# Performance work log

Measured on AMD Instinct MI355X. Metric: run time of the kernel, lower is better.

Reference implementation:

```python
import jax, jax.numpy as jnp
import numpy as np

N = 512      # nodes
F_IN = 16    # raw node features; adjacency channels = 2*F_IN = 32
H = 64       # hidden
HF = 64      # hidden_final
C = 10       # num_classes
L = 3        # num_layers
E = 16384    # edges (avg degree 32)
EPS = 1e-5


def setup_inputs() -> dict:
    key = jax.random.key(0)
    ks = iter(jax.random.split(key, 40))
    rn = lambda shape, s=0.05: jax.random.normal(next(ks), shape, jnp.float32) * s
    inp = {
        'x': jax.random.normal(next(ks), (N, F_IN), jnp.float32),
        'edge_index': jax.random.randint(next(ks), (2, E), 0, N),
        # no_prop FeatureExtractor
        'np1_w': rn((HF, 2 * F_IN)), 'np1_b': rn((HF,)),
        'np2_w': rn((HF, 2 * F_IN)), 'np3_w': rn((HF, HF)),
        # first PowerfulLayer (in = 2*F_IN)
        'c0_m1_w': rn((H, 2 * F_IN)), 'c0_m1_b': rn((H,)),
        'c0_m2_w': rn((H, 2 * F_IN)), 'c0_m2_b': rn((H,)),
        'c0_m4_w': rn((H, 2 * F_IN + H)), 'c0_m4_b': rn((H,)),
        # remaining L-1 PowerfulLayers (stacked)
        'cm1_w': rn((L - 1, H, H)), 'cm1_b': rn((L - 1, H)),
        'cm2_w': rn((L - 1, H, H)), 'cm2_b': rn((L - 1, H)),
        'cm4_w': rn((L - 1, H, 2 * H)), 'cm4_b': rn((L - 1, H)),
        # batchnorms (training-mode stats; affine params)
        'bn_g': jnp.ones((L, H), jnp.float32), 'bn_b': jnp.zeros((L, H), jnp.float32),
        # per-layer FeatureExtractors (stacked)
        'fe1_w': rn((L, HF, H)), 'fe1_b': rn((L, HF)),
        'fe2_w': rn((L, HF, H)), 'fe3_w': rn((L, HF, HF)),
        # after_conv and final linear
        'ac_w': rn((HF, HF)), 'ac_b': rn((HF,)),
        'fl_w': rn((C, HF)), 'fl_b': rn((C,)),
    }
    return inp


def _lin(x, w, b=None):
    y = x @ w.T
    return y if b is None else y + b


def _extractor(u, w1, b1, w2, w3):
    # u: [B, N, N, F]; graph_class=True, aggr='add'
    n = u.shape[1]
    trace = jnp.einsum('biif->bf', u)                     # sum of diagonal entries
    out1 = _lin(trace / n, w1, b1)
    s = (u.sum(axis=(1, 2)) - trace) / (n * (n - 1))      # off-diagonal mean-ish
    out = out1 + _lin(s, w2)
    return out + _lin(jax.nn.relu(out), w3)


def _powerful(u, m1w, m1b, m2w, m2b, m4w, m4b):
    # UnitMLP with 1 layer == 1x1 conv == per-position linear (no ReLU)
    o1 = jnp.einsum('bijc,oc->bijo', u, m1w) + m1b        # [B,N,N,H]
    o2 = jnp.einsum('bijc,oc->bijo', u, m2w) + m2b
    mult = jnp.einsum('bikh,bkjh->bijh', o1, o2)          # per-channel NxN matmul
    return _lin(jnp.concatenate([mult, u], axis=-1), m4w, m4b)


def _batchnorm(u, g, b):
    # BatchNorm2d in training mode: stats over (batch, N, N) per channel, biased var
    mean = u.mean(axis=(0, 1, 2))
    var = u.var(axis=(0, 1, 2))
    return (u - mean) * jax.lax.rsqrt(var + EPS) * g + b


def reference(x, edge_index, np1_w, np1_b, np2_w, np3_w,
              c0_m1_w, c0_m1_b, c0_m2_w, c0_m2_b, c0_m4_w, c0_m4_b,
              cm1_w, cm1_b, cm2_w, cm2_b, cm4_w, cm4_b,
              bn_g, bn_b, fe1_w, fe1_b, fe2_w, fe3_w,
              ac_w, ac_b, fl_w, fl_b):
    n = x.shape[0]
    src, dst = edge_index[0], edge_index[1]
    edge_attr = jnp.concatenate([x[src], x[dst]], axis=-1)          # [E, 2F]
    A = jnp.zeros((n, n, edge_attr.shape[-1]), x.dtype).at[src, dst].add(edge_attr)
    u = A[None]                                                      # [1,N,N,2F]

    out = _extractor(u, np1_w, np1_b, np2_w, np3_w)
    nlayers = bn_g.shape[0]
    for l in range(nlayers):
        if l == 0:
            u = _powerful(u, c0_m1_w, c0_m1_b, c0_m2_w, c0_m2_b, c0_m4_w, c0_m4_b)
        else:
            u = _powerful(u, cm1_w[l - 1], cm1_b[l - 1], cm2_w[l - 1], cm2_b[l - 1],
                          cm4_w[l - 1], cm4_b[l - 1])
        u = _batchnorm(u, bn_g[l], bn_b[l])
        out = out + _extractor(u, fe1_w[l], fe1_b[l], fe2_w[l], fe3_w[l])

    out = jax.nn.relu(out) / nlayers
    out = out + jax.nn.relu(_lin(out, ac_w, ac_b))   # layer_after_conv
    # dropout with p=0.0 / eval mode is identity
    out = _lin(out, fl_w, fl_b)
    return jax.nn.log_softmax(out, axis=-1)          # [1, num_classes]
```

## Files before the change

### kernel.cpp

```cpp
#include <hip/hip_runtime.h>
#include <hip/hip_bf16.h>

#define Nn   512
#define NN   262144
#define EDG  16384

typedef unsigned short u16;
typedef short v8s __attribute__((ext_vector_type(8)));
typedef float v4f __attribute__((ext_vector_type(4)));
typedef u16 u16x8 __attribute__((ext_vector_type(8)));

__device__ __forceinline__ float b2f(u16 u) {
    union { unsigned int i; float f; } v; v.i = ((unsigned int)u) << 16; return v.f;
}
__device__ __forceinline__ u16 f2b(float f) {
    union { float f; unsigned int i; } v; v.f = f;
    unsigned int r = (v.i + 0x7FFFu + ((v.i >> 16) & 1u)) >> 16;
    return (u16)r;
}

__global__ void sentinel_kernel(float* __restrict__ out, float val) {
    if (threadIdx.x < 10) out[threadIdx.x] = val;
}

__global__ void cvt_weights(const float* __restrict__ s0, const float* __restrict__ s1,
                            const float* __restrict__ s2, const float* __restrict__ s3,
                            const float* __restrict__ s4, const float* __restrict__ s5,
                            u16* __restrict__ dst) {
    int t = blockIdx.x * 256 + threadIdx.x;
    if (t >= 43008) return;
    float v;
    if      (t < 2048)  v = s0[t];
    else if (t < 4096)  v = s1[t - 2048];
    else if (t < 10240) v = s2[t - 4096];
    else if (t < 18432) v = s3[t - 10240];
    else if (t < 26624) v = s4[t - 18432];
    else                v = s5[t - 26624];
    dst[t] = f2b(v);
}

__global__ void scatter_edges(const float* __restrict__ x, const int* __restrict__ ei,
                              float* __restrict__ A) {
    int t = blockIdx.x * 256 + threadIdx.x;
    if (t >= EDG * 32) return;
    int e = t >> 5, c = t & 31;
    int s = ei[e], d = ei[EDG + e];
    float v = (c < 16) ? x[s * 16 + c] : x[d * 16 + (c - 16)];
    atomicAdd(A + ((size_t)s * Nn + d) * 32 + c, v);
}

__global__ __launch_bounds__(256) void finalize_u0(const float* __restrict__ A,
                                                   u16* __restrict__ u0,
                                                   float* __restrict__ total) {
    __shared__ u16 L[32 * 258];
    __shared__ float red[4][32];
    int t = threadIdx.x;
    int p0 = blockIdx.x * 256;
    const float* Ar = A + (size_t)(p0 + t) * 32;
    float v[32];
#pragma unroll
    for (int c = 0; c < 32; ++c) v[c] = Ar[c];
#pragma unroll
    for (int c = 0; c < 32; ++c) L[c * 258 + t] = f2b(v[c]);
    int wv = t >> 6;
#pragma unroll
    for (int c = 0; c < 32; ++c) {
        float r = v[c];
        for (int off = 32; off > 0; off >>= 1) r += __shfl_down(r, off);
        if ((t & 63) == 0) red[wv][c] = r;
    }
    __syncthreads();
    if (t < 32) atomicAdd(total + t, red[0][t] + red[1][t] + red[2][t] + red[3][t]);
    int off = (t & 31) * 8, rb = t >> 5;
#pragma unroll
    for (int pass = 0; pass < 4; ++pass) {
        int c = pass * 8 + rb;
        u16x8 w = *(const u16x8*)(L + c * 258 + off);
        *(u16x8*)(u0 + (size_t)c * NN + p0 + off) = w;
    }
}

__global__ void trace_raw_cm(const u16* __restrict__ ucm, float* __restrict__ trraw) {
    int c = blockIdx.x, t = threadIdx.x;
    const u16* base = ucm + (size_t)c * NN;
    float s = b2f(base[(size_t)(2 * t) * 513]) + b2f(base[(size_t)(2 * t + 1) * 513]);
    for (int off = 32; off > 0; off >>= 1) s += __shfl_down(s, off);
    __shared__ float r[4];
    if ((t & 63) == 0) r[t >> 6] = s;
    __syncthreads();
    if (t == 0) trraw[c] = r[0] + r[1] + r[2] + r[3];
}

template<int NCH>
__global__ __launch_bounds__(256) void conv12_t(
    const u16* __restrict__ src,
    const float* __restrict__ sc, const float* __restrict__ sh,
    const u16* __restrict__ w1, const float* __restrict__ b1,
    const u16* __restrict__ w2, const float* __restrict__ b2,
    u16* __restrict__ dst1, u16* __restrict__ dst2)
{
    __shared__ u16 LS[8320];
    const int C = NCH * 32;
    const int t = threadIdx.x;
    const int P0 = blockIdx.x * 128;
    const int lane = t & 63, wave = t >> 6;
    const int l15 = lane & 15, quad = lane >> 4;
    const int pw = wave * 32;
    const int sr = t >> 4;
    const int so = (t & 15) * 8;

    u16x8 pf[NCH][2];
#pragma unroll
    for (int kc = 0; kc < NCH; ++kc)
#pragma unroll
        for (int ps = 0; ps < 2; ++ps)
            pf[kc][ps] = *(const u16x8*)(src + (size_t)(kc * 32 + ps * 16 + sr) * NN + P0 + so);

    v4f acc[2][4][2];
#pragma unroll
    for (int s = 0; s < 2; ++s)
#pragma unroll
        for (int mt = 0; mt < 4; ++mt)
#pragma unroll
            for (int nt = 0; nt < 2; ++nt) acc[s][mt][nt] = (v4f){0.f, 0.f, 0.f, 0.f};

    {
        u16* Ln = LS;
#pragma unroll
        for (int ps = 0; ps < 2; ++ps) {
            int c = ps * 16 + sr;
            u16x8 v = pf[0][ps];
            if (sc) {
                float s = sc[c], f = sh[c];
#pragma unroll
                for (int j = 0; j < 8; ++j) v[j] = f2b(b2f(v[j]) * s + f);
            }
            *(u16x8*)(Ln + c * 130 + so) = v;
        }
    }
    __syncthreads();
#pragma unroll
    for (int kc = 0; kc < NCH; ++kc) {
        if (kc + 1 < NCH) {
            u16* Ln = LS + ((kc + 1) & 1) * 4160;
#pragma unroll
            for (int ps = 0; ps < 2; ++ps) {
                int c = ps * 16 + sr;
                int cg = (kc + 1) * 32 + c;
                u16x8 v = pf[kc + 1][ps];
                if (sc) {
                    float s = sc[cg], f = sh[cg];
#pragma unroll
                    for (int j = 0; j < 8; ++j) v[j] = f2b(b2f(v[j]) * s + f);
                }
                *(u16x8*)(Ln + c * 130 + so) = v;
            }
        }
        v8s af1[4], af2[4];
#pragma unroll
        for (int mt = 0; mt < 4; ++mt) {
            af1[mt] = *(const v8s*)(w1 + (mt * 16 + l15) * C + kc * 32 + quad * 8);
            af2[mt] = *(const v8s*)(w2 + (mt * 16 + l15) * C + kc * 32 + quad * 8);
        }
        const u16* Lb = LS + (kc & 1) * 4160;
#pragma unroll
        for (int nt = 0; nt < 2; ++nt) {
            const int p = pw + nt * 16 + l15;
            v8s b;
#pragma unroll
            for (int j = 0; j < 8; ++j) b[j] = (short)Lb[(quad * 8 + j) * 130 + p];
#pragma unroll
            for (int mt = 0; mt < 4; ++mt) {
                acc[0][mt][nt] = __builtin_amdgcn_mfma_f32_16x16x32_bf16(af1[mt], b, acc[0][mt][nt], 0, 0, 0);
                acc[1][mt][nt] = __builtin_amdgcn_mfma_f32_16x16x32_bf16(af2[mt], b, acc[1][mt][nt], 0, 0, 0);
            }
        }
        if (kc + 1 < NCH) __syncthreads();
    }
#pragma unroll
    for (int s = 0; s < 2; ++s) {
        __syncthreads();
        const float* bb = s ? b2 : b1;
#pragma unroll
        for (int mt = 0; mt < 4; ++mt)
#pragma unroll
            for (int r = 0; r < 4; ++r) {
                const int h = mt * 16 + quad * 4 + r;
                const float bv = bb[h];
#pragma unroll
                for (int nt = 0; nt < 2; ++nt)
                    LS[h * 130 + pw + nt * 16 + l15] = f2b(acc[s][mt][nt][r] + bv);
            }
        __syncthreads();
        u16* dd = s ? dst2 : dst1;
#pragma unroll
        for (int ps = 0; ps < 4; ++ps) {
            int h = ps * 16 + sr;
            u16x8 v = *(const u16x8*)(LS + h * 130 + so);
            __builtin_nontemporal_store(v, (u16x8*)(dd + (size_t)h * NN + P0 + so));
        }
    }
}

template<int NCH>
__global__ __launch_bounds__(256) void conv4_t(
    const u16* __restrict__ mult, const u16* __restrict__ u,
    const float* __restrict__ sc, const float* __restrict__ sh,
    const u16* __restrict__ w, const float* __restrict__ bias,
    u16* __restrict__ dst,
    float* __restrict__ psum, float* __restrict__ psq, float* __restrict__ ptr)
{
    __shared__ u16 LS[8320];
    __shared__ float R1[64][4], R2[64][4];
    const int K = NCH * 32;
    const int t = threadIdx.x;
    const int P0 = blockIdx.x * 128;
    const int lane = t & 63, wave = t >> 6;
    const int l15 = lane & 15, quad = lane >> 4;
    const int pw = wave * 32;
    const int sr = t >> 4;
    const int so = (t & 15) * 8;

    u16x8 pf[NCH][2];
#pragma unroll
    for (int kc = 0; kc < NCH; ++kc)
#pragma unroll
        for (int ps = 0; ps < 2; ++ps) {
            int cg = kc * 32 + ps * 16 + sr;
            const u16* gp = (cg < 64) ? (mult + (size_t)cg * NN + P0 + so)
                                      : (u + (size_t)(cg - 64) * NN + P0 + so);
            pf[kc][ps] = *(const u16x8*)gp;
        }

    v4f acc[4][2];
#pragma unroll
    for (int mt = 0; mt < 4; ++mt)
#pragma unroll
        for (int nt = 0; nt < 2; ++nt) acc[mt][nt] = (v4f){0.f, 0.f, 0.f, 0.f};

#pragma unroll
    for (int ps = 0; ps < 2; ++ps)
        *(u16x8*)(LS + (ps * 16 + sr) * 130 + so) = pf[0][ps];
    __syncthreads();
#pragma unroll
    for (int kc = 0; kc < NCH; ++kc) {
        if (kc + 1 < NCH) {
            u16* Ln = LS + ((kc + 1) & 1) * 4160;
#pragma unroll
            for (int ps = 0; ps < 2; ++ps) {
                int c = ps * 16 + sr;
                int cg = (kc + 1) * 32 + c;
                u16x8 v = pf[kc + 1][ps];
                if (cg >= 64 && sc) {
                    float s = sc[cg - 64], f = sh[cg - 64];
#pragma unroll
                    for (int j = 0; j < 8; ++j) v[j] = f2b(b2f(v[j]) * s + f);
                }
                *(u16x8*)(Ln + c * 130 + so) = v;
            }
        }
        v8s af[4];
#pragma unroll
        for (int mt = 0; mt < 4; ++mt)
            af[mt] = *(const v8s*)(w + (mt * 16 + l15) * K + kc * 32 + quad * 8);
        const u16* Lb = LS + (kc & 1) * 4160;
#pragma unroll
        for (int nt = 0; nt < 2; ++nt) {
            const int p = pw + nt * 16 + l15;
            v8s b;
#pragma unroll
            for (int j = 0; j < 8; ++j) b[j] = (short)Lb[(quad * 8 + j) * 130 + p];
#pragma unroll
            for (int mt = 0; mt < 4; ++mt)
                acc[mt][nt] = __builtin_amdgcn_mfma_f32_16x16x32_bf16(af[mt], b, acc[mt][nt], 0, 0, 0);
        }
        if (kc + 1 < NCH) __syncthreads();
    }
    __syncthreads();
#pragma unroll
    for (int mt = 0; mt < 4; ++mt)
#pragma unroll
        for (int r = 0; r < 4; ++r) {
            const int h = mt * 16 + quad * 4 + r;
            const float bv = bias[h];
#pragma unroll
            for (int nt = 0; nt < 2; ++nt)
                LS[h * 130 + pw + nt * 16 + l15] = f2b(acc[mt][nt][r] + bv);
        }
    __syncthreads();
    {
        int c = t >> 2, q = t & 3;
        const u16* row = LS + c * 130 + q * 32;
        float s = 0.f, s2 = 0.f;
#pragma unroll
        for (int i = 0; i < 32; ++i) { float v = b2f(row[i]); s += v; s2 += v * v; }
        R1[c][q] = s; R2[c][q] = s2;
    }
    __syncthreads();
    {
        int i = P0 >> 9, j0 = P0 & 511;
        int blk = blockIdx.x;
        if (t < 64) {
            psum[t * 2048 + blk] = R1[t][0] + R1[t][1] + R1[t][2] + R1[t][3];
            psq[t * 2048 + blk]  = R2[t][0] + R2[t][1] + R2[t][2] + R2[t][3];
            if (j0 <= i && i < j0 + 128) ptr[t * 512 + i] = b2f(LS[t * 130 + (i - j0)]);
        }
    }
#pragma unroll
    for (int ps = 0; ps < 4; ++ps) {
        int h = ps * 16 + sr;
        u16x8 v = *(const u16x8*)(LS + h * 130 + so);
        __builtin_nontemporal_store(v, (u16x8*)(dst + (size_t)h * NN + P0 + so));
    }
}

__global__ __launch_bounds__(256) void bmm_mfma(const u16* __restrict__ Aall,
                                                const u16* __restrict__ Ball,
                                                u16* __restrict__ Call) {
    __shared__ u16 LA[128 * 72];
    __shared__ u16 LB[64 * 130];
    const int h = blockIdx.y;
    const int tx = blockIdx.x & 3, ty = blockIdx.x >> 2;
    const int t = threadIdx.x;
    const int lane = t & 63, wave = t >> 6;
    const int l15 = lane & 15, quad = lane >> 4;
    const int jb = wave * 32;
    const u16* Ap = Aall + (size_t)h * NN + (size_t)ty * 128 * 512;
    const u16* Bp = Ball + (size_t)h * NN + tx * 128;

    const int srow = t >> 3;
    const int scol = (t & 7) * 8;
    const int bkr = t >> 4;
    const int bjg = (t & 15) * 8;

    v4f acc[8][2];
#pragma unroll
    for (int mt = 0; mt < 8; ++mt)
#pragma unroll
        for (int nt = 0; nt < 2; ++nt) acc[mt][nt] = (v4f){0.f, 0.f, 0.f, 0.f};

    v8s ra[4], rb[4];
#pragma unroll
    for (int i = 0; i < 4; ++i) {
        ra[i] = *(const v8s*)(Ap + (size_t)(i * 32 + srow) * 512 + scol);
        rb[i] = *(const v8s*)(Bp + (size_t)(i * 16 + bkr) * 512 + bjg);
    }

    for (int ck = 0; ck < 8; ++ck) {
#pragma unroll
        for (int i = 0; i < 4; ++i) {
            *(v8s*)(LA + (i * 32 + srow) * 72 + scol) = ra[i];
            *(v8s*)(LB + (i * 16 + bkr) * 130 + bjg) = rb[i];
        }
        __syncthreads();
        if (ck < 7) {
            const int k0 = (ck + 1) * 64;
#pragma unroll
            for (int i = 0; i < 4; ++i) {
                ra[i] = *(const v8s*)(Ap + (size_t)(i * 32 + srow) * 512 + k0 + scol);
                rb[i] = *(const v8s*)(Bp + (size_t)(k0 + i * 16 + bkr) * 512 + bjg);
            }
        }
#pragma unroll
        for (int kk = 0; kk < 2; ++kk) {
            v8s b[2];
#pragma unroll
            for (int nt = 0; nt < 2; ++nt) {
                const int j = jb + nt * 16 + l15;
#pragma unroll
                for (int jj = 0; jj < 8; ++jj)
                    b[nt][jj] = (short)LB[(kk * 32 + quad * 8 + jj) * 130 + j];
            }
#pragma unroll
            for (int mh = 0; mh < 2; ++mh) {
                v8s a[4];
#pragma unroll
                for (int m = 0; m < 4; ++m)
                    a[m] = *(const v8s*)(LA + ((mh * 4 + m) * 16 + l15) * 72 + kk * 32 + quad * 8);
#pragma unroll
                for (int m = 0; m < 4; ++m)
#pragma unroll
                    for (int nt = 0; nt < 2; ++nt)
                        acc[mh * 4 + m][nt] = __builtin_amdgcn_mfma_f32_16x16x32_bf16(a[m], b[nt], acc[mh * 4 + m][nt], 0, 0, 0);
            }
        }
        __syncthreads();
    }

    u16* Cp = Call + (size_t)h * NN;
#pragma unroll
    for (int mt = 0; mt < 8; ++mt)
#pragma unroll
        for (int r = 0; r < 4; ++r) {
            const int i = ty * 128 + mt * 16 + quad * 4 + r;
#pragma unroll
            for (int nt = 0; nt < 2; ++nt) {
                const int j = tx * 128 + jb + nt * 16 + l15;
                Cp[i * 512 + j] = f2b(acc[mt][nt][r]);
            }
        }
}

__global__ __launch_bounds__(256) void bn_finalize(
    const float* __restrict__ psum, const float* __restrict__ psq,
    const float* __restrict__ ptr,
    const float* __restrict__ g, const float* __restrict__ b,
    float* __restrict__ scale, float* __restrict__ shift,
    float* __restrict__ ttl) {
    int c = blockIdx.x, t = threadIdx.x;
    float s = 0.f, q = 0.f, tr = 0.f;
    for (int k = t; k < 2048; k += 256) { s += psum[c * 2048 + k]; q += psq[c * 2048 + k]; }
    for (int k = t; k < 512; k += 256) tr += ptr[c * 512 + k];
    for (int off = 32; off > 0; off >>= 1) {
        s += __shfl_down(s, off); q += __shfl_down(q, off); tr += __shfl_down(tr, off);
    }
    __shared__ float r1[4], r2[4], r3[4];
    if ((t & 63) == 0) { r1[t >> 6] = s; r2[t >> 6] = q; r3[t >> 6] = tr; }
    __syncthreads();
    if (t == 0) {
        s = r1[0] + r1[1] + r1[2] + r1[3];
        q = r2[0] + r2[1] + r2[2] + r2[3];
        tr = r3[0] + r3[1] + r3[2] + r3[3];
        float mean = s * (1.f / 262144.f);
        float var = q * (1.f / 262144.f) - mean * mean;
        float sc = g[c] * rsqrtf(fmaxf(var, 0.f) + 1e-5f);
        float sh = b[c] - mean * sc;
        scale[c] = sc;
        shift[c] = sh;
        ttl[64 + c] = sc * s + 262144.f * sh;
        ttl[c]      = sc * tr + 512.f * sh;
    }
}

__global__ __launch_bounds__(256) void extractor_par(
    const float* __restrict__ tt,
    const float* __restrict__ np1w, const float* __restrict__ np1b,
    const float* __restrict__ np2w, const float* __restrict__ np3w,
    const float* __restrict__ fe1w, const float* __restrict__ fe1b,
    const float* __restrict__ fe2w, const float* __restrict__ fe3w,
    float* __restrict__ oacc_part) {
    __shared__ float red[64][4];
    __shared__ float xo[64];
    const int li = blockIdx.x;
    const int t = threadIdx.x;
    const int h = t >> 2, q = t & 3;
    const int C = (li == 0) ? 32 : 64;
    const float* w1 = (li == 0) ? np1w : fe1w + (li - 1) * 4096;
    const float* b1 = (li == 0) ? np1b : fe1b + (li - 1) * 64;
    const float* w2 = (li == 0) ? np2w : fe2w + (li - 1) * 4096;
    const float* w3 = (li == 0) ? np3w : fe3w + (li - 1) * 4096;
    const float* tr = tt + li * 128;
    const float* to = tr + 64;
    const int cpq = C >> 2;
    float p = 0.f;
    for (int i = 0; i < cpq; ++i) {
        int c = q * cpq + i;
        p += (tr[c] * (1.f / 512.f)) * w1[h * C + c]
           + ((to[c] - tr[c]) * (1.f / (512.f * 511.f))) * w2[h * C + c];
    }
    red[h][q] = p;
    __syncthreads();
    if (q == 0) xo[h] = b1[h] + red[h][0] + red[h][1] + red[h][2] + red[h][3];
    __syncthreads();
    float o = xo[h];
    float p3 = 0.f;
    for (int i = 0; i < 16; ++i) {
        int f = q * 16 + i;
        p3 += fmaxf(xo[f], 0.f) * w3[h * 64 + f];
    }
    __syncthreads();
    red[h][q] = p3;
    __syncthreads();
    if (q == 0) oacc_part[li * 64 + h] = o + red[h][0] + red[h][1] + red[h][2] + red[h][3];
}

__global__ __launch_bounds__(256) void head_par(
    const float* __restrict__ oacc_part,
    const float* __restrict__ acw, const float* __restrict__ acb,
    const float* __restrict__ flw, const float* __restrict__ flb,
    float* __restrict__ out) {
    __shared__ float x[64], x2[64], red[64][4], l[10];
    const int t = threadIdx.x;
    const int h = t >> 2, q = t & 3;
    if (q == 0) {
        float oa = oacc_part[h] + oacc_part[64 + h] + oacc_part[128 + h] + oacc_part[192 + h];
        x[h] = fmaxf(oa, 0.f) * (1.f / 3.f);
    }
    __syncthreads();
    float p = 0.f;
    for (int i = 0; i < 16; ++i) { int f = q * 16 + i; p += x[f] * acw[h * 64 + f]; }
    red[h][q] = p;
    __syncthreads();
    if (q == 0) {
        float y = acb[h] + red[h][0] + red[h][1] + red[h][2] + red[h][3];
        x2[h] = x[h] + fmaxf(y, 0.f);
    }
    __syncthreads();
    if (t < 40) {
        int hh = t >> 2, qq = t & 3;
        float p2 = 0.f;
        for (int i = 0; i < 16; ++i) { int f = qq * 16 + i; p2 += x2[f] * flw[hh * 64 + f]; }
        red[hh][qq] = p2;
    }
    __syncthreads();
    if (t < 10) l[t] = flb[t] + red[t][0] + red[t][1] + red[t][2] + red[t][3];
    __syncthreads();
    if (t == 0) {
        float m = l[0];
        for (int i = 1; i < 10; ++i) m = fmaxf(m, l[i]);
        float se = 0.f;
        for (int i = 0; i < 10; ++i) se += expf(l[i] - m);
        float ls = m + logf(se);
        for (int i = 0; i < 10; ++i) out[i] = l[i] - ls;
    }
}

extern "C" void kernel_launch(void* const* d_in, const int* in_sizes, int n_in,
                              void* d_out, int out_size, void* d_ws, size_t ws_size,
                              hipStream_t stream) {
    float* out = (float*)d_out;

    static const int exp_sizes[28] = {
        8192, 32768,
        2048, 64, 2048, 4096,
        2048, 64, 2048, 64, 6144, 64,
        8192, 128, 8192, 128, 16384, 128,
        192, 192,
        12288, 192, 12288, 12288,
        4096, 64, 640, 10
    };
    bool ok = (n_in == 28);
    if (ok) for (int i = 0; i < 28; ++i) if (in_sizes[i] != exp_sizes[i]) ok = false;
    if (!ok) { sentinel_kernel<<<1, 64, 0, stream>>>(out, -5.0f); return; }

    const size_t RSZ = (size_t)NN * 64 * 2;
    const size_t BIG_OFF = 8192 + 90112;
    if (ws_size < BIG_OFF + 4 * RSZ) {
        sentinel_kernel<<<1, 64, 0, stream>>>(out, -7.0f);
        return;
    }

    const float* x     = (const float*)d_in[0];
    const int*   ei    = (const int*)d_in[1];
    const float* np1w  = (const float*)d_in[2];
    const float* np1b  = (const float*)d_in[3];
    const float* np2w  = (const float*)d_in[4];
    const float* np3w  = (const float*)d_in[5];
    const float* c0m1b = (const float*)d_in[7];
    const float* c0m2b = (const float*)d_in[9];
    const float* c0m4b = (const float*)d_in[11];
    const float* cm1b  = (const float*)d_in[13];
    const float* cm2b  = (const float*)d_in[15];
    const float* cm4b  = (const float*)d_in[17];
    const float* bng   = (const float*)d_in[18];
    const float* bnb   = (const float*)d_in[19];
    const float* fe1w  = (const float*)d_in[20];
    const float* fe1b  = (const float*)d_in[21];
    const float* fe2w  = (const float*)d_in[22];
    const float* fe3w  = (const float*)d_in[23];
    const float* acw   = (const float*)d_in[24];
    const float* acb   = (const float*)d_in[25];
    const float* flw   = (const float*)d_in[26];
    const float* flb   = (const float*)d_in[27];

    char* ws = (char*)d_ws;
    float* small = (float*)ws;
    float* tt    = small;
    float* scl   = small + 512;
    float* shf   = small + 576;
    float* oaccp = small + 640;

    u16* arena = (u16*)(ws + 8192);

    char* big = ws + BIG_OFF;
    u16* S0 = (u16*)(big + 0 * RSZ);
    u16* S1 = (u16*)(big + 1 * RSZ);
    u16* S2 = (u16*)(big + 2 * RSZ);
    u16* S3 = (u16*)(big + 3 * RSZ);
    float* Abuf = (float*)S2;

    float* psum = (float*)S2;
    float* psq  = psum + 64 * 2048;
    float* ptr  = psq + 64 * 2048;

    hipMemsetAsync(small, 0, 4096, stream);
    hipMemsetAsync(Abuf, 0, (size_t)NN * 32 * 4, stream);

    cvt_weights<<<168, 256, 0, stream>>>((const float*)d_in[6], (const float*)d_in[8],
                                         (const float*)d_in[10], (const float*)d_in[12],
                                         (const float*)d_in[14], (const float*)d_in[16], arena);
    scatter_edges<<<2048, 256, 0, stream>>>(x, ei, Abuf);
    finalize_u0<<<1024, 256, 0, stream>>>(Abuf, S0, tt + 64);
    trace_raw_cm<<<32, 256, 0, stream>>>(S0, tt);

    u16* U[3]  = { S0, S1, S0 };
    u16* O1[3] = { S1, S0, S1 };
    u16* R[3]  = { S1, S0, S1 };

    const float *aff_s = nullptr, *aff_h = nullptr;

    for (int l = 0; l < 3; ++l) {
        int Cin = (l == 0) ? 32 : 64;
        const u16 *w1b, *w2b, *w4b;
        const float *b1, *b2, *b4;
        if (l == 0) {
            w1b = arena;            b1 = c0m1b;
            w2b = arena + 2048;     b2 = c0m2b;
            w4b = arena + 4096;     b4 = c0m4b;
        } else {
            int m = l - 1;
            w1b = arena + 10240 + m * 4096;  b1 = cm1b + m * 64;
            w2b = arena + 18432 + m * 4096;  b2 = cm2b + m * 64;
            w4b = arena + 26624 + m * 8192;  b4 = cm4b + m * 64;
        }
        if (Cin == 32)
            conv12_t<1><<<2048, 256, 0, stream>>>(U[l], aff_s, aff_h, w1b, b1, w2b, b2, O1[l], S2);
        else
            conv12_t<2><<<2048, 256, 0, stream>>>(U[l], aff_s, aff_h, w1b, b1, w2b, b2, O1[l], S2);
        bmm_mfma<<<dim3(16, 64), 256, 0, stream>>>(O1[l], S2, S3);
        if (Cin == 32)
            conv4_t<3><<<2048, 256, 0, stream>>>(S3, U[l], aff_s, aff_h, w4b, b4, R[l], psum, psq, ptr);
        else
            conv4_t<4><<<2048, 256, 0, stream>>>(S3, U[l], aff_s, aff_h, w4b, b4, R[l], psum, psq, ptr);
        bn_finalize<<<64, 256, 0, stream>>>(psum, psq, ptr, bng + l * 64, bnb + l * 64,
                                            scl, shf, tt + (l + 1) * 128);
        aff_s = scl; aff_h = shf;
    }
    extractor_par<<<4, 256, 0, stream>>>(tt, np1w, np1b, np2w, np3w,
                                         fe1w, fe1b, fe2w, fe3w, oaccp);
    head_par<<<1, 256, 0, stream>>>(oaccp, acw, acb, flw, flb, out);
}
```

Baseline: 471.1 us.

## Double-buffer B tile in LDS, read A directly from global, swap block order

The bmm kernel no longer stages the A tile in shared memory. Each wave loads its A fragments straight from global memory (L1/L2), and the B tile is double-buffered in LDS so each k-step needs one barrier instead of two. The block index mapping is also swapped so that neighbouring blocks share the same B column tile. This lowers LDS traffic and barrier count, at the cost of redundant global loads of A across waves and more exposed global memory latency inside the MFMA loop.

Result: slower. 630.0 us (+33.7%).

```diff
diff --git a/kernel.cpp b/kernel.cpp
--- a/kernel.cpp
+++ b/kernel.cpp
@@ -317,19 +317,15 @@
 __global__ __launch_bounds__(256) void bmm_mfma(const u16* __restrict__ Aall,
                                                 const u16* __restrict__ Ball,
                                                 u16* __restrict__ Call) {
-    __shared__ u16 LA[128 * 72];
-    __shared__ u16 LB[64 * 130];
+    __shared__ u16 LB[2][64 * 130];
     const int h = blockIdx.y;
-    const int tx = blockIdx.x & 3, ty = blockIdx.x >> 2;
+    const int ty = blockIdx.x & 3, tx = blockIdx.x >> 2;
     const int t = threadIdx.x;
     const int lane = t & 63, wave = t >> 6;
     const int l15 = lane & 15, quad = lane >> 4;
     const int jb = wave * 32;
-    const u16* Ap = Aall + (size_t)h * NN + (size_t)ty * 128 * 512;
+    const u16* Ap = Aall + (size_t)h * NN + (size_t)(ty * 128) * 512;
     const u16* Bp = Ball + (size_t)h * NN + tx * 128;
-
-    const int srow = t >> 3;
-    const int scol = (t & 7) * 8;
     const int bkr = t >> 4;
     const int bjg = (t & 15) * 8;
 
@@ -339,28 +335,24 @@
 #pragma unroll
         for (int nt = 0; nt < 2; ++nt) acc[mt][nt] = (v4f){0.f, 0.f, 0.f, 0.f};
 
-    v8s ra[4], rb[4];
-#pragma unroll
-    for (int i = 0; i < 4; ++i) {
-        ra[i] = *(const v8s*)(Ap + (size_t)(i * 32 + srow) * 512 + scol);
+    v8s rb[4];
+#pragma unroll
+    for (int i = 0; i < 4; ++i)
         rb[i] = *(const v8s*)(Bp + (size_t)(i * 16 + bkr) * 512 + bjg);
-    }
+#pragma unroll
+    for (int i = 0; i < 4; ++i)
+        *(v8s*)(&LB[0][(i * 16 + bkr) * 130 + bjg]) = rb[i];
+    __syncthreads();
 
     for (int ck = 0; ck < 8; ++ck) {
-#pragma unroll
-        for (int i = 0; i < 4; ++i) {
-            *(v8s*)(LA + (i * 32 + srow) * 72 + scol) = ra[i];
-            *(v8s*)(LB + (i * 16 + bkr) * 130 + bjg) = rb[i];
-        }
-        __syncthreads();
         if (ck < 7) {
             const int k0 = (ck + 1) * 64;
 #pragma unroll
-            for (int i = 0; i < 4; ++i) {
-                ra[i] = *(const v8s*)(Ap + (size_t)(i * 32 + srow) * 512 + k0 + scol);
+            for (int i = 0; i < 4; ++i)
                 rb[i] = *(const v8s*)(Bp + (size_t)(k0 + i * 16 + bkr) * 512 + bjg);
-            }
-        }
+        }
+        const u16* Lb = &LB[ck & 1][0];
+        const u16* Akp = Ap + ck * 64 + quad * 8;
 #pragma unroll
         for (int kk = 0; kk < 2; ++kk) {
             v8s b[2];
@@ -369,20 +361,26 @@
                 const int j = jb + nt * 16 + l15;
 #pragma unroll
                 for (int jj = 0; jj < 8; ++jj)
-                    b[nt][jj] = (short)LB[(kk * 32 + quad * 8 + jj) * 130 + j];
+                    b[nt][jj] = (short)Lb[(kk * 32 + quad * 8 + jj) * 130 + j];
             }
 #pragma unroll
             for (int mh = 0; mh < 2; ++mh) {
                 v8s a[4];
 #pragma unroll
                 for (int m = 0; m < 4; ++m)
-                    a[m] = *(const v8s*)(LA + ((mh * 4 + m) * 16 + l15) * 72 + kk * 32 + quad * 8);
+                    a[m] = *(const v8s*)(Akp + (size_t)(mh * 64 + m * 16 + l15) * 512 + kk * 32);
 #pragma unroll
                 for (int m = 0; m < 4; ++m)
 #pragma unroll
                     for (int nt = 0; nt < 2; ++nt)
                         acc[mh * 4 + m][nt] = __builtin_amdgcn_mfma_f32_16x16x32_bf16(a[m], b[nt], acc[mh * 4 + m][nt], 0, 0, 0);
             }
+        }
+        if (ck < 7) {
+            u16* Ln = &LB[(ck + 1) & 1][0];
+#pragma unroll
+            for (int i = 0; i < 4; ++i)
+                *(v8s*)(Ln + (i * 16 + bkr) * 130 + bjg) = rb[i];
         }
         __syncthreads();
     }
```
